# Optimization experiments

Hardware: AMD Instinct MI355X
Metric: run time of the kernel (lower is better)

Reference implementation:

```python
import jax, jax.numpy as jnp
import numpy as np

B, T, C, NH = 8, 512, 512, 8
HD = C // NH

def _layernorm(x, g, b, eps=1e-5):
    mu = jnp.mean(x, axis=-1, keepdims=True)
    var = jnp.var(x, axis=-1, keepdims=True)
    return (x - mu) * jax.lax.rsqrt(var + eps) * g + b

def setup_inputs() -> dict:
    key = jax.random.key(0)
    ks = jax.random.split(key, 5)
    return {
        "x": jax.random.normal(ks[0], (B, T, C), jnp.float32),
        "w_attn": jax.random.normal(ks[1], (3 * C, C), jnp.float32) * (1.0 / np.sqrt(C)),
        "b_attn": jnp.zeros((3 * C,), jnp.float32),
        "w_proj": jax.random.normal(ks[2], (C, C), jnp.float32) * (1.0 / np.sqrt(C)),
        "b_proj": jnp.zeros((C,), jnp.float32),
        "q_gamma": jnp.ones((C,), jnp.float32),
        "q_beta": jnp.zeros((C,), jnp.float32),
        "k_gamma": jnp.ones((C,), jnp.float32),
        "k_beta": jnp.zeros((C,), jnp.float32),
        "rel_emb": jax.random.normal(ks[3], (T, C), jnp.float32) * 0.02,
    }

def reference(x, w_attn, b_attn, w_proj, b_proj, q_gamma, q_beta, k_gamma, k_beta, rel_emb):
    b, t, c = x.shape
    # QKV projection (torch Linear: x @ W.T + b)
    qkv = x @ w_attn.T + b_attn                       # [B,T,3C]
    q, k, v = jnp.split(qkv, 3, axis=-1)
    # per-stream LayerNorm over full embedding dim (q_ln/k_ln = LayerNorm(n_embd))
    q = _layernorm(q, q_gamma, q_beta)
    k = _layernorm(k, k_gamma, k_beta)
    # split heads -> [B,NH,T,HD]
    q = q.reshape(b, t, NH, HD).transpose(0, 2, 1, 3)
    k = k.reshape(b, t, NH, HD).transpose(0, 2, 1, 3)
    v = v.reshape(b, t, NH, HD).transpose(0, 2, 1, 3)
    # relative-position bias: gather rel_emb[|i-j|] -> [T,T,NH,HD]
    idx = jnp.abs(jnp.arange(t)[None, :] - jnp.arange(t)[:, None])  # [T,T] int
    rel = rel_emb[idx].reshape(t, t, NH, HD)
    rel_bias = jnp.einsum("bhqd,qkhd->bhqk", q, rel)  # [B,NH,T,T]
    scale = 1.0 / np.sqrt(HD)
    scores = (jnp.einsum("bhqd,bhkd->bhqk", q, k) + rel_bias) * scale
    causal = jnp.tril(jnp.ones((t, t), bool))
    scores = jnp.where(causal[None, None], scores, jnp.finfo(scores.dtype).min)
    att = jax.nn.softmax(scores, axis=-1)
    y = jnp.einsum("bhqk,bhkd->bhqd", att, v)         # [B,NH,T,HD]
    y = y.transpose(0, 2, 1, 3).reshape(b, t, c)
    return y @ w_proj.T + b_proj
```

## Files before the change

### kernel.cpp

```cpp
#include <hip/hip_runtime.h>
#include <hip/hip_bf16.h>
#include <cstddef>

#define BB 8
#define TT 512
#define CC 512
#define NHH 8
#define HDD 64

typedef __attribute__((ext_vector_type(8))) short short8;
typedef __attribute__((ext_vector_type(4))) float f32x4;

__device__ __forceinline__ unsigned short f2bf(float f) {
    unsigned u = __float_as_uint(f);
    u += 0x7FFFu + ((u >> 16) & 1u);
    return (unsigned short)(u >> 16);
}
__device__ __forceinline__ float bf2f(unsigned short h) {
    return __uint_as_float(((unsigned)h) << 16);
}

__global__ __launch_bounds__(256) void cvt_all_k(
    const float* __restrict__ x, const float* __restrict__ wa,
    const float* __restrict__ wp, const float* __restrict__ rel,
    unsigned short* __restrict__ Xb, unsigned short* __restrict__ Wqb,
    unsigned short* __restrict__ Wpb, unsigned short* __restrict__ Relb)
{
    const int bidx = blockIdx.x;
    const float* in;
    unsigned short* out;
    int base;
    if (bidx < 2048)      { in = x;   out = Xb;   base = bidx; }
    else if (bidx < 2816) { in = wa;  out = Wqb;  base = bidx - 2048; }
    else if (bidx < 3072) { in = wp;  out = Wpb;  base = bidx - 2816; }
    else                  { in = rel; out = Relb; base = bidx - 3072; }
    const int i = base * 1024 + threadIdx.x * 4;
    const float4 v = *(const float4*)(in + i);
    unsigned short tmp[4] = {f2bf(v.x), f2bf(v.y), f2bf(v.z), f2bf(v.w)};
    *(uint2*)(out + i) = *(const uint2*)tmp;
}

__global__ __launch_bounds__(256, 2) void gemm_qkv_mfma(
    const unsigned short* __restrict__ Xb, const unsigned short* __restrict__ Wb,
    const float* __restrict__ bias, unsigned short* __restrict__ qkbuf,
    unsigned short* __restrict__ VT)
{
    __shared__ __align__(16) unsigned short lds[128 * 136];

    const int tid = threadIdx.x;
    const int w = tid >> 6, lane = tid & 63;
    const int c = lane & 15, quad = lane >> 4;
    const int wm = w >> 1, wn = w & 1;
    const int bm = blockIdx.y * 128, bn = blockIdx.x * 128;

    const unsigned short* pp[8];
#pragma unroll
    for (int l = 0; l < 8; ++l) {
        const int ci = w * 8 + l;
        if (ci < 16) {
            const int m16 = ci >> 1, kk = ci & 1;
            pp[l] = Xb + (size_t)(bm + m16 * 16 + c) * 512 + kk * 32 + quad * 8;
        } else {
            const int cb = ci - 16, n16 = cb >> 1, kk = cb & 1;
            pp[l] = Wb + (size_t)(bn + n16 * 16 + c) * 512 + kk * 32 + quad * 8;
        }
    }

    f32x4 acc[4][4];
#pragma unroll
    for (int i = 0; i < 4; ++i)
#pragma unroll
        for (int j = 0; j < 4; ++j) acc[i][j] = (f32x4){0.f, 0.f, 0.f, 0.f};

    short8 pre[8];
#pragma unroll
    for (int l = 0; l < 8; ++l) pre[l] = *(const short8*)pp[l];

    for (int k0 = 0; k0 < 512; k0 += 64) {
        __syncthreads();
#pragma unroll
        for (int l = 0; l < 8; ++l)
            *(short8*)&lds[(w * 8 + l) * 512 + lane * 8] = pre[l];
        __syncthreads();
        if (k0 + 64 < 512) {
#pragma unroll
            for (int l = 0; l < 8; ++l)
                pre[l] = *(const short8*)(pp[l] + k0 + 64);
        }
#pragma unroll
        for (int kk = 0; kk < 2; ++kk) {
            short8 af[4], bfr[4];
#pragma unroll
            for (int i = 0; i < 4; ++i)
                af[i] = *(const short8*)&lds[((wm * 4 + i) * 2 + kk) * 512 + lane * 8];
#pragma unroll
            for (int j = 0; j < 4; ++j)
                bfr[j] = *(const short8*)&lds[(16 + (wn * 4 + j) * 2 + kk) * 512 + lane * 8];
#pragma unroll
            for (int i = 0; i < 4; ++i)
#pragma unroll
                for (int j = 0; j < 4; ++j)
                    acc[i][j] = __builtin_amdgcn_mfma_f32_16x16x32_bf16(
                        af[i], bfr[j], acc[i][j], 0, 0, 0);
        }
    }

    float bj[4];
#pragma unroll
    for (int j = 0; j < 4; ++j) bj[j] = bias[bn + wn * 64 + j * 16 + c];

    if (bn < 1024) {
#pragma unroll
        for (int i = 0; i < 4; ++i)
#pragma unroll
            for (int j = 0; j < 4; ++j) {
                const int n = bn + wn * 64 + j * 16 + c;
#pragma unroll
                for (int r = 0; r < 4; ++r) {
                    const int m = bm + wm * 64 + i * 16 + quad * 4 + r;
                    qkbuf[(size_t)m * 1024 + n] = f2bf(acc[i][j][r] + bj[j]);
                }
            }
    } else {
        __syncthreads();
#pragma unroll
        for (int i = 0; i < 4; ++i)
#pragma unroll
            for (int j = 0; j < 4; ++j) {
                const int col = wn * 64 + j * 16 + c;
                const int row0 = wm * 64 + i * 16 + quad * 4;
                unsigned short t4[4];
#pragma unroll
                for (int r = 0; r < 4; ++r) t4[r] = f2bf(acc[i][j][r] + bj[j]);
                *(uint2*)&lds[col * 136 + row0] = *(const uint2*)t4;
            }
        __syncthreads();
        const int bi = bm >> 9, tb = bm & 511;
        const int hd0 = bn - 1024;
#pragma unroll
        for (int l = 0; l < 8; ++l) {
            const int idx = l * 256 + tid;
            const int col = idx >> 4, grp = idx & 15;
            const short8 v = *(const short8*)&lds[col * 136 + grp * 8];
            const int hd = hd0 + col, h = hd >> 6, d = hd & 63;
            *(short8*)(VT + ((size_t)(bi * NHH + h) * HDD + d) * TT + tb + grp * 8) = v;
        }
    }
}

__global__ __launch_bounds__(256) void ln_k(
    const unsigned short* __restrict__ qkbuf,
    const float* __restrict__ qg, const float* __restrict__ qb,
    const float* __restrict__ kg, const float* __restrict__ kb,
    unsigned short* __restrict__ Qh, unsigned short* __restrict__ Kh)
{
    const int wv = threadIdx.x >> 6, lane = threadIdx.x & 63;
    const int row = blockIdx.x * 4 + wv;
    const int bi = row >> 9, t = row & 511;
    const unsigned short* base = qkbuf + (size_t)row * 1024;

#pragma unroll
    for (int s = 0; s < 2; ++s) {
        const short8 v8 = *(const short8*)(base + s * 512 + lane * 8);
        float vf[8];
#pragma unroll
        for (int i = 0; i < 8; ++i) vf[i] = bf2f(((const unsigned short*)&v8)[i]);
        float sum = 0.f, sq = 0.f;
#pragma unroll
        for (int i = 0; i < 8; ++i) { sum += vf[i]; sq += vf[i] * vf[i]; }
#pragma unroll
        for (int off = 1; off < 64; off <<= 1) {
            sum += __shfl_xor(sum, off);
            sq += __shfl_xor(sq, off);
        }
        const float mu = sum * (1.f / 512.f);
        const float var = sq * (1.f / 512.f) - mu * mu;
        const float rsg = rsqrtf(var + 1e-5f);
        const float* gam = (s ? kg : qg) + lane * 8;
        const float* bet = (s ? kb : qb) + lane * 8;
        const float4 g0 = *(const float4*)gam, g1 = *(const float4*)(gam + 4);
        const float4 b0 = *(const float4*)bet, b1 = *(const float4*)(bet + 4);
        const float gv[8] = {g0.x, g0.y, g0.z, g0.w, g1.x, g1.y, g1.z, g1.w};
        const float bv[8] = {b0.x, b0.y, b0.z, b0.w, b1.x, b1.y, b1.z, b1.w};
        const float osc = s ? 1.0f : 0.125f;
        unsigned short o8[8];
#pragma unroll
        for (int i = 0; i < 8; ++i)
            o8[i] = f2bf(((vf[i] - mu) * rsg * gv[i] + bv[i]) * osc);
        unsigned short* outp = s ? Kh : Qh;
        *(short8*)(outp + ((size_t)(bi * NHH + (lane >> 3)) * TT + t) * HDD
                   + (lane & 7) * 8) = *(const short8*)o8;
    }
}

#define RD_BODY(nr_)                                                            \
    {                                                                           \
        const short8 br0 = *(const short8*)&Rels[((nr_) * 2 + 0) * 512 + lane * 8]; \
        const short8 br1 = *(const short8*)&Rels[((nr_) * 2 + 1) * 512 + lane * 8]; \
        f32x4 a2 = (f32x4){0.f, 0.f, 0.f, 0.f};                                 \
        a2 = __builtin_amdgcn_mfma_f32_16x16x32_bf16(aq0, br0, a2, 0, 0, 0);    \
        a2 = __builtin_amdgcn_mfma_f32_16x16x32_bf16(aq1, br1, a2, 0, 0, 0);    \
        const int colw = (mbase + (nr_) * 16 + c) & 127;                        \
        _Pragma("unroll")                                                       \
        for (int r = 0; r < 4; ++r)                                             \
            RDs[w][(quad * 4 + r) * 132 + colw] = f2bf(a2[r]);                  \
    }

__global__ __launch_bounds__(256, 2) void attn_k(
    const unsigned short* __restrict__ Qh, const unsigned short* __restrict__ Kh,
    const unsigned short* __restrict__ VT, const unsigned short* __restrict__ Relb,
    unsigned short* __restrict__ Yb)
{
    __shared__ __align__(16) unsigned short Ks[8 * 512];
    __shared__ __align__(16) unsigned short Vs[8 * 512];
    __shared__ __align__(16) unsigned short Rels[16 * 512];
    __shared__ __align__(16) unsigned short Ps[4][16 * 72];
    __shared__ __align__(16) unsigned short RDs[4][16 * 132];

    const int tid = threadIdx.x;
    const int w = tid >> 6;
    const int lane = tid & 63;
    const int c = lane & 15;
    const int quad = lane >> 4;

    const int bid = blockIdx.x;
    const int bit0 = bid & 1, bit8 = (bid >> 8) & 1;
    const int s_ = bit0 ^ bit8;
    const int q0 = (bid >> 1) & 7;
    const int qt = s_ ? 7 - q0 : q0;
    const int h = (bid >> 4) & 7;
    const int b = ((bid >> 7) & 1) | (bit8 << 1) | (bit0 << 2);
    const int i0 = qt * 64;

    const unsigned short* Qbase = Qh + (size_t)(b * NHH + h) * TT * HDD;
    const unsigned short* Kbase = Kh + (size_t)(b * NHH + h) * TT * HDD;
    const unsigned short* Vbase = VT + (size_t)(b * NHH + h) * HDD * TT;
    const unsigned short* Rbase = Relb + h * HDD;

    const unsigned short* qp = Qbase + (size_t)(i0 + w * 16 + c) * HDD + quad * 8;
    const short8 aq0 = *(const short8*)qp;
    const short8 aq1 = *(const short8*)(qp + 32);

#pragma unroll
    for (int kk = 0; kk < 2; ++kk) {
        const unsigned short* gp = Kbase + (size_t)(w * 16 + c) * HDD + kk * 32 + quad * 8;
        *(short8*)&Ks[(w * 2 + kk) * 512 + lane * 8] = *(const short8*)gp;
    }
#pragma unroll
    for (int js = 0; js < 2; ++js) {
        const unsigned short* gp = Vbase + (size_t)(w * 16 + c) * TT + js * 32 + quad * 8;
        *(short8*)&Vs[(w * 2 + js) * 512 + lane * 8] = *(const short8*)gp;
    }
    {
        const int mb0 = i0 - 63;
#pragma unroll
        for (int sb = 0; sb < 2; ++sb) {
#pragma unroll
            for (int kk = 0; kk < 2; ++kk) {
                const int n16 = w * 2 + sb;
                int mrow = mb0 + n16 * 16 + c;
                mrow = mrow < 0 ? 0 : (mrow > 511 ? 511 : mrow);
                *(short8*)&Rels[(n16 * 2 + kk) * 512 + lane * 8] =
                    *(const short8*)(Rbase + (size_t)mrow * CC + kk * 32 + quad * 8);
            }
        }
    }

    f32x4 oacc[4];
    float m_i[4], l_i[4];
#pragma unroll
    for (int r = 0; r < 4; ++r) { m_i[r] = -1e30f; l_i[r] = 0.f; }
#pragma unroll
    for (int nd = 0; nd < 4; ++nd) oacc[nd] = (f32x4){0.f, 0.f, 0.f, 0.f};

    __syncthreads();

    for (int jt = 0; jt <= qt; ++jt) {
        const int j0 = jt * 64;

        short8 pK0, pK1, pV0, pV1, pR0, pR1;
        if (jt < qt) {
            const int j1 = j0 + 64;
            const unsigned short* kp = Kbase + (size_t)(j1 + w * 16 + c) * HDD + quad * 8;
            pK0 = *(const short8*)kp;
            pK1 = *(const short8*)(kp + 32);
            const unsigned short* vp = Vbase + (size_t)(w * 16 + c) * TT + j1 + quad * 8;
            pV0 = *(const short8*)vp;
            pV1 = *(const short8*)(vp + 32);
            int mr = i0 - j1 - 63 + w * 16 + c;
            mr = mr < 0 ? 0 : (mr > 511 ? 511 : mr);
            const unsigned short* rp = Rbase + (size_t)mr * CC + quad * 8;
            pR0 = *(const short8*)rp;
            pR1 = *(const short8*)(rp + 32);
        }

        f32x4 sAcc[4];
#pragma unroll
        for (int ns = 0; ns < 4; ++ns) {
            const short8 bk0 = *(const short8*)&Ks[(ns * 2 + 0) * 512 + lane * 8];
            const short8 bk1 = *(const short8*)&Ks[(ns * 2 + 1) * 512 + lane * 8];
            f32x4 a2 = (f32x4){0.f, 0.f, 0.f, 0.f};
            a2 = __builtin_amdgcn_mfma_f32_16x16x32_bf16(aq0, bk0, a2, 0, 0, 0);
            a2 = __builtin_amdgcn_mfma_f32_16x16x32_bf16(aq1, bk1, a2, 0, 0, 0);
            sAcc[ns] = a2;
        }
        const int mbase = i0 - j0 - 63;
        if (jt == 0) {
#pragma unroll
            for (int nr = 0; nr < 8; ++nr) RD_BODY(nr)
        } else {
#pragma unroll
            for (int nr = 0; nr < 4; ++nr) RD_BODY(nr)
        }

        const int dbase = i0 - j0;
        float sc[4][4];
#pragma unroll
        for (int ns = 0; ns < 4; ++ns) {
#pragma unroll
            for (int r = 0; r < 4; ++r) {
                const int r16 = quad * 4 + r;
                const int jc = ns * 16 + c;
                const int dp = (dbase + w * 16 + r16 - jc) & 127;
                const float rdv = bf2f(RDs[w][r16 * 132 + dp]);
                sc[ns][r] = sAcc[ns][r] + rdv;
            }
        }
        if (jt == qt) {
#pragma unroll
            for (int ns = 0; ns < 4; ++ns)
#pragma unroll
                for (int r = 0; r < 4; ++r)
                    if (ns * 16 + c > w * 16 + quad * 4 + r) sc[ns][r] = -1e30f;
        }

        float alpha[4];
#pragma unroll
        for (int r = 0; r < 4; ++r) {
            float m = fmaxf(fmaxf(sc[0][r], sc[1][r]), fmaxf(sc[2][r], sc[3][r]));
#pragma unroll
            for (int off = 1; off < 16; off <<= 1) m = fmaxf(m, __shfl_xor(m, off));
            const float mn = fmaxf(m_i[r], m);
            alpha[r] = __expf(m_i[r] - mn);
            m_i[r] = mn;
        }
        float rs[4] = {0.f, 0.f, 0.f, 0.f};
#pragma unroll
        for (int ns = 0; ns < 4; ++ns) {
#pragma unroll
            for (int r = 0; r < 4; ++r) {
                const float p = __expf(sc[ns][r] - m_i[r]);
                rs[r] += p;
                Ps[w][(quad * 4 + r) * 72 + ns * 16 + c] = f2bf(p);
            }
        }
#pragma unroll
        for (int r = 0; r < 4; ++r) {
#pragma unroll
            for (int off = 1; off < 16; off <<= 1) rs[r] += __shfl_xor(rs[r], off);
            l_i[r] = l_i[r] * alpha[r] + rs[r];
        }
#pragma unroll
        for (int nd = 0; nd < 4; ++nd)
#pragma unroll
            for (int r = 0; r < 4; ++r) oacc[nd][r] *= alpha[r];

        const short8 ap0 = *(const short8*)&Ps[w][c * 72 + 0 * 32 + quad * 8];
        const short8 ap1 = *(const short8*)&Ps[w][c * 72 + 1 * 32 + quad * 8];
#pragma unroll
        for (int nd = 0; nd < 4; ++nd) {
            const short8 bv0 = *(const short8*)&Vs[(nd * 2 + 0) * 512 + lane * 8];
            const short8 bv1 = *(const short8*)&Vs[(nd * 2 + 1) * 512 + lane * 8];
            oacc[nd] = __builtin_amdgcn_mfma_f32_16x16x32_bf16(ap0, bv0, oacc[nd], 0, 0, 0);
            oacc[nd] = __builtin_amdgcn_mfma_f32_16x16x32_bf16(ap1, bv1, oacc[nd], 0, 0, 0);
        }

        if (jt < qt) {
            __syncthreads();
#pragma unroll
            for (int kk = 0; kk < 2; ++kk)
                *(short8*)&Ks[(w * 2 + kk) * 512 + lane * 8] = (kk ? pK1 : pK0);
#pragma unroll
            for (int js = 0; js < 2; ++js)
                *(short8*)&Vs[(w * 2 + js) * 512 + lane * 8] = (js ? pV1 : pV0);
#pragma unroll
            for (int kk = 0; kk < 2; ++kk)
                *(short8*)&Rels[(w * 2 + kk) * 512 + lane * 8] = (kk ? pR1 : pR0);
            __syncthreads();
        }
    }

#pragma unroll
    for (int r = 0; r < 4; ++r) {
        const float inv = 1.f / l_i[r];
        const int trow = i0 + w * 16 + quad * 4 + r;
        unsigned short* yb = Yb + ((size_t)b * TT + trow) * CC + h * HDD;
#pragma unroll
        for (int nd = 0; nd < 4; ++nd)
            yb[nd * 16 + c] = f2bf(oacc[nd][r] * inv);
    }
}

__global__ __launch_bounds__(256, 2) void gemm_proj_mfma(
    const unsigned short* __restrict__ Yb, const unsigned short* __restrict__ Wp,
    const float* __restrict__ bias, float* __restrict__ out)
{
    __shared__ __align__(16) unsigned short lds[24 * 512];

    const int tid = threadIdx.x;
    const int w = tid >> 6, lane = tid & 63;
    const int c = lane & 15, quad = lane >> 4;
    const int wm = w >> 1, wn = w & 1;
    const int bm = blockIdx.y * 64, bn = blockIdx.x * 128;

    const unsigned short* pp[6];
#pragma unroll
    for (int l = 0; l < 6; ++l) {
        const int ci = w * 6 + l;
        if (ci < 8) {
            const int m16 = ci >> 1, kk = ci & 1;
            pp[l] = Yb + (size_t)(bm + m16 * 16 + c) * 512 + kk * 32 + quad * 8;
        } else {
            const int cb = ci - 8, n16 = cb >> 1, kk = cb & 1;
            pp[l] = Wp + (size_t)(bn + n16 * 16 + c) * 512 + kk * 32 + quad * 8;
        }
    }

    f32x4 acc[2][4];
#pragma unroll
    for (int i = 0; i < 2; ++i)
#pragma unroll
        for (int j = 0; j < 4; ++j) acc[i][j] = (f32x4){0.f, 0.f, 0.f, 0.f};

    short8 pre[6];
#pragma unroll
    for (int l = 0; l < 6; ++l) pre[l] = *(const short8*)pp[l];

    for (int k0 = 0; k0 < 512; k0 += 64) {
        __syncthreads();
#pragma unroll
        for (int l = 0; l < 6; ++l)
            *(short8*)&lds[(w * 6 + l) * 512 + lane * 8] = pre[l];
        __syncthreads();
        if (k0 + 64 < 512) {
#pragma unroll
            for (int l = 0; l < 6; ++l)
                pre[l] = *(const short8*)(pp[l] + k0 + 64);
        }
#pragma unroll
        for (int kk = 0; kk < 2; ++kk) {
            short8 af[2], bfr[4];
#pragma unroll
            for (int i = 0; i < 2; ++i)
                af[i] = *(const short8*)&lds[((wm * 2 + i) * 2 + kk) * 512 + lane * 8];
#pragma unroll
            for (int j = 0; j < 4; ++j)
                bfr[j] = *(const short8*)&lds[(8 + (wn * 4 + j) * 2 + kk) * 512 + lane * 8];
#pragma unroll
            for (int i = 0; i < 2; ++i)
#pragma unroll
                for (int j = 0; j < 4; ++j)
                    acc[i][j] = __builtin_amdgcn_mfma_f32_16x16x32_bf16(
                        af[i], bfr[j], acc[i][j], 0, 0, 0);
        }
    }

#pragma unroll
    for (int j = 0; j < 4; ++j) {
        const int n = bn + wn * 64 + j * 16 + c;
        const float bj = bias[n];
#pragma unroll
        for (int i = 0; i < 2; ++i)
#pragma unroll
            for (int r = 0; r < 4; ++r) {
                const int m = bm + wm * 32 + i * 16 + quad * 4 + r;
                out[(size_t)m * 512 + n] = acc[i][j][r] + bj;
            }
    }
}

extern "C" void kernel_launch(void* const* d_in, const int* in_sizes, int n_in,
                              void* d_out, int out_size, void* d_ws, size_t ws_size,
                              hipStream_t stream)
{
    const float* x      = (const float*)d_in[0];
    const float* w_attn = (const float*)d_in[1];
    const float* b_attn = (const float*)d_in[2];
    const float* w_proj = (const float*)d_in[3];
    const float* b_proj = (const float*)d_in[4];
    const float* q_g    = (const float*)d_in[5];
    const float* q_b    = (const float*)d_in[6];
    const float* k_g    = (const float*)d_in[7];
    const float* k_b    = (const float*)d_in[8];
    const float* rel    = (const float*)d_in[9];
    float* out = (float*)d_out;

    unsigned short* qkbuf = (unsigned short*)d_ws;
    unsigned short* Qh   = qkbuf + (size_t)4096 * 1024;
    unsigned short* Kh   = Qh + (size_t)4096 * 512;
    unsigned short* VT   = Kh + (size_t)4096 * 512;
    unsigned short* Relb = VT + (size_t)4096 * 512;
    unsigned short* Xb   = Relb + (size_t)512 * 512;
    unsigned short* Wqb  = Xb + (size_t)4096 * 512;
    unsigned short* Wpb  = Wqb + (size_t)1536 * 512;
    unsigned short* Yb   = qkbuf;

    cvt_all_k<<<3328, 256, 0, stream>>>(x, w_attn, w_proj, rel, Xb, Wqb, Wpb, Relb);
    gemm_qkv_mfma<<<dim3(12, 32), 256, 0, stream>>>(Xb, Wqb, b_attn, qkbuf, VT);
    ln_k<<<1024, 256, 0, stream>>>(qkbuf, q_g, q_b, k_g, k_b, Qh, Kh);
    attn_k<<<512, 256, 0, stream>>>(Qh, Kh, VT, Relb, Yb);
    gemm_proj_mfma<<<dim3(4, 64), 256, 0, stream>>>(Yb, Wpb, b_proj, out);
}
```

Measured before the change: 139.5 us.

## Fuse all stages into one cooperative persistent kernel with grid syncs

Merges the five launches (convert, QKV GEMM, layernorm, attention, projection) into one cooperative kernel of 512 blocks, with grid.sync between stages and a shared LDS buffer reused across stages. The aim is to remove per-launch overhead and the gaps between kernels. It also folds log2(e) into the Q scale so softmax can use exp2f. Risks: grid-wide barriers, idle blocks in stages with fewer tiles, higher register and LDS pressure from one fused kernel, and a fallback path if the cooperative launch fails.

```diff
diff --git a/kernel.cpp b/kernel.cpp
--- a/kernel.cpp
+++ b/kernel.cpp
@@ -1,6 +1,9 @@
 #include <hip/hip_runtime.h>
 #include <hip/hip_bf16.h>
+#include <hip/hip_cooperative_groups.h>
 #include <cstddef>
+
+namespace cg = cooperative_groups;
 
 #define BB 8
 #define TT 512
@@ -20,13 +23,14 @@
     return __uint_as_float(((unsigned)h) << 16);
 }
 
-__global__ __launch_bounds__(256) void cvt_all_k(
+
+__device__ __forceinline__ void cvt_body(
+    int bidx, int tid,
     const float* __restrict__ x, const float* __restrict__ wa,
     const float* __restrict__ wp, const float* __restrict__ rel,
     unsigned short* __restrict__ Xb, unsigned short* __restrict__ Wqb,
     unsigned short* __restrict__ Wpb, unsigned short* __restrict__ Relb)
 {
-    const int bidx = blockIdx.x;
     const float* in;
     unsigned short* out;
     int base;
@@ -34,24 +38,22 @@
     else if (bidx < 2816) { in = wa;  out = Wqb;  base = bidx - 2048; }
     else if (bidx < 3072) { in = wp;  out = Wpb;  base = bidx - 2816; }
     else                  { in = rel; out = Relb; base = bidx - 3072; }
-    const int i = base * 1024 + threadIdx.x * 4;
+    const int i = base * 1024 + tid * 4;
     const float4 v = *(const float4*)(in + i);
     unsigned short tmp[4] = {f2bf(v.x), f2bf(v.y), f2bf(v.z), f2bf(v.w)};
     *(uint2*)(out + i) = *(const uint2*)tmp;
 }
 
-__global__ __launch_bounds__(256, 2) void gemm_qkv_mfma(
+__device__ __forceinline__ void qkv_body(
+    int bx, int by, int tid, unsigned short* __restrict__ lds,
     const unsigned short* __restrict__ Xb, const unsigned short* __restrict__ Wb,
     const float* __restrict__ bias, unsigned short* __restrict__ qkbuf,
     unsigned short* __restrict__ VT)
 {
-    __shared__ __align__(16) unsigned short lds[128 * 136];
-
-    const int tid = threadIdx.x;
     const int w = tid >> 6, lane = tid & 63;
     const int c = lane & 15, quad = lane >> 4;
     const int wm = w >> 1, wn = w & 1;
-    const int bm = blockIdx.y * 128, bn = blockIdx.x * 128;
+    const int bm = by * 128, bn = bx * 128;
 
     const unsigned short* pp[8];
 #pragma unroll
@@ -148,14 +150,15 @@
     }
 }
 
-__global__ __launch_bounds__(256) void ln_k(
+__device__ __forceinline__ void ln_body(
+    int vblk, int tid,
     const unsigned short* __restrict__ qkbuf,
     const float* __restrict__ qg, const float* __restrict__ qb,
     const float* __restrict__ kg, const float* __restrict__ kb,
     unsigned short* __restrict__ Qh, unsigned short* __restrict__ Kh)
 {
-    const int wv = threadIdx.x >> 6, lane = threadIdx.x & 63;
-    const int row = blockIdx.x * 4 + wv;
+    const int wv = tid >> 6, lane = tid & 63;
+    const int row = vblk * 4 + wv;
     const int bi = row >> 9, t = row & 511;
     const unsigned short* base = qkbuf + (size_t)row * 1024;
 
@@ -182,7 +185,7 @@
         const float4 b0 = *(const float4*)bet, b1 = *(const float4*)(bet + 4);
         const float gv[8] = {g0.x, g0.y, g0.z, g0.w, g1.x, g1.y, g1.z, g1.w};
         const float bv[8] = {b0.x, b0.y, b0.z, b0.w, b1.x, b1.y, b1.z, b1.w};
-        const float osc = s ? 1.0f : 0.125f;
+        const float osc = s ? 1.0f : 0.125f * 1.44269504088896f;
         unsigned short o8[8];
 #pragma unroll
         for (int i = 0; i < 8; ++i)
@@ -203,27 +206,26 @@
         const int colw = (mbase + (nr_) * 16 + c) & 127;                        \
         _Pragma("unroll")                                                       \
         for (int r = 0; r < 4; ++r)                                             \
-            RDs[w][(quad * 4 + r) * 132 + colw] = f2bf(a2[r]);                  \
-    }
-
-__global__ __launch_bounds__(256, 2) void attn_k(
+            RDs[w * 2112 + (quad * 4 + r) * 132 + colw] = f2bf(a2[r]);          \
+    }
+
+__device__ __forceinline__ void attn_body(
+    int bid, int tid, unsigned short* __restrict__ sm,
     const unsigned short* __restrict__ Qh, const unsigned short* __restrict__ Kh,
     const unsigned short* __restrict__ VT, const unsigned short* __restrict__ Relb,
     unsigned short* __restrict__ Yb)
 {
-    __shared__ __align__(16) unsigned short Ks[8 * 512];
-    __shared__ __align__(16) unsigned short Vs[8 * 512];
-    __shared__ __align__(16) unsigned short Rels[16 * 512];
-    __shared__ __align__(16) unsigned short Ps[4][16 * 72];
-    __shared__ __align__(16) unsigned short RDs[4][16 * 132];
-
-    const int tid = threadIdx.x;
+    unsigned short* Ks   = sm;
+    unsigned short* Vs   = sm + 4096;
+    unsigned short* Rels = sm + 8192;
+    unsigned short* Ps   = sm + 16384;
+    unsigned short* RDs  = sm + 20992;
+
     const int w = tid >> 6;
     const int lane = tid & 63;
     const int c = lane & 15;
     const int quad = lane >> 4;
 
-    const int bid = blockIdx.x;
     const int bit0 = bid & 1, bit8 = (bid >> 8) & 1;
     const int s_ = bit0 ^ bit8;
     const int q0 = (bid >> 1) & 7;
@@ -322,7 +324,7 @@
                 const int r16 = quad * 4 + r;
                 const int jc = ns * 16 + c;
                 const int dp = (dbase + w * 16 + r16 - jc) & 127;
-                const float rdv = bf2f(RDs[w][r16 * 132 + dp]);
+                const float rdv = bf2f(RDs[w * 2112 + r16 * 132 + dp]);
                 sc[ns][r] = sAcc[ns][r] + rdv;
             }
         }
@@ -341,7 +343,7 @@
 #pragma unroll
             for (int off = 1; off < 16; off <<= 1) m = fmaxf(m, __shfl_xor(m, off));
             const float mn = fmaxf(m_i[r], m);
-            alpha[r] = __expf(m_i[r] - mn);
+            alpha[r] = exp2f(m_i[r] - mn);
             m_i[r] = mn;
         }
         float rs[4] = {0.f, 0.f, 0.f, 0.f};
@@ -349,9 +351,9 @@
         for (int ns = 0; ns < 4; ++ns) {
 #pragma unroll
             for (int r = 0; r < 4; ++r) {
-                const float p = __expf(sc[ns][r] - m_i[r]);
+                const float p = exp2f(sc[ns][r] - m_i[r]);
                 rs[r] += p;
-                Ps[w][(quad * 4 + r) * 72 + ns * 16 + c] = f2bf(p);
+                Ps[w * 1152 + (quad * 4 + r) * 72 + ns * 16 + c] = f2bf(p);
             }
         }
 #pragma unroll
@@ -365,8 +367,8 @@
 #pragma unroll
             for (int r = 0; r < 4; ++r) oacc[nd][r] *= alpha[r];
 
-        const short8 ap0 = *(const short8*)&Ps[w][c * 72 + 0 * 32 + quad * 8];
-        const short8 ap1 = *(const short8*)&Ps[w][c * 72 + 1 * 32 + quad * 8];
+        const short8 ap0 = *(const short8*)&Ps[w * 1152 + c * 72 + 0 * 32 + quad * 8];
+        const short8 ap1 = *(const short8*)&Ps[w * 1152 + c * 72 + 1 * 32 + quad * 8];
 #pragma unroll
         for (int nd = 0; nd < 4; ++nd) {
             const short8 bv0 = *(const short8*)&Vs[(nd * 2 + 0) * 512 + lane * 8];
@@ -401,17 +403,15 @@
     }
 }
 
-__global__ __launch_bounds__(256, 2) void gemm_proj_mfma(
+__device__ __forceinline__ void proj_body(
+    int bx, int by, int tid, unsigned short* __restrict__ lds,
     const unsigned short* __restrict__ Yb, const unsigned short* __restrict__ Wp,
     const float* __restrict__ bias, float* __restrict__ out)
 {
-    __shared__ __align__(16) unsigned short lds[24 * 512];
-
-    const int tid = threadIdx.x;
     const int w = tid >> 6, lane = tid & 63;
     const int c = lane & 15, quad = lane >> 4;
     const int wm = w >> 1, wn = w & 1;
-    const int bm = blockIdx.y * 64, bn = blockIdx.x * 128;
+    const int bm = by * 64, bn = bx * 128;
 
     const unsigned short* pp[6];
 #pragma unroll
@@ -477,6 +477,86 @@
                 out[(size_t)m * 512 + n] = acc[i][j][r] + bj;
             }
     }
+}
+
+__global__ __launch_bounds__(256, 2) void mega_k(
+    const float* __restrict__ x, const float* __restrict__ wa,
+    const float* __restrict__ ba, const float* __restrict__ wp,
+    const float* __restrict__ bp,
+    const float* __restrict__ qg, const float* __restrict__ qb,
+    const float* __restrict__ kg, const float* __restrict__ kb,
+    const float* __restrict__ rel, float* __restrict__ out,
+    unsigned short* __restrict__ qkbuf, unsigned short* __restrict__ Qh,
+    unsigned short* __restrict__ Kh, unsigned short* __restrict__ VT,
+    unsigned short* __restrict__ Relb, unsigned short* __restrict__ Xb,
+    unsigned short* __restrict__ Wqb, unsigned short* __restrict__ Wpb)
+{
+    __shared__ __align__(16) unsigned short SM[29440];
+    cg::grid_group grid = cg::this_grid();
+    const int bid = blockIdx.x;
+    const int tid = threadIdx.x;
+
+    for (int v = bid; v < 3328; v += 512)
+        cvt_body(v, tid, x, wa, wp, rel, Xb, Wqb, Wpb, Relb);
+    grid.sync();
+
+    if (bid < 384)
+        qkv_body(bid % 12, bid / 12, tid, SM, Xb, Wqb, ba, qkbuf, VT);
+    grid.sync();
+
+    for (int v = bid; v < 1024; v += 512)
+        ln_body(v, tid, qkbuf, qg, qb, kg, kb, Qh, Kh);
+    grid.sync();
+
+    attn_body(bid, tid, SM, Qh, Kh, VT, Relb, qkbuf );
+    grid.sync();
+
+    if (bid < 256)
+        proj_body(bid & 3, bid >> 2, tid, SM, qkbuf , Wpb, bp, out);
+}
+
+__global__ __launch_bounds__(256) void cvt_all_k(
+    const float* __restrict__ x, const float* __restrict__ wa,
+    const float* __restrict__ wp, const float* __restrict__ rel,
+    unsigned short* __restrict__ Xb, unsigned short* __restrict__ Wqb,
+    unsigned short* __restrict__ Wpb, unsigned short* __restrict__ Relb)
+{
+    cvt_body(blockIdx.x, threadIdx.x, x, wa, wp, rel, Xb, Wqb, Wpb, Relb);
+}
+
+__global__ __launch_bounds__(256, 2) void gemm_qkv_mfma(
+    const unsigned short* __restrict__ Xb, const unsigned short* __restrict__ Wb,
+    const float* __restrict__ bias, unsigned short* __restrict__ qkbuf,
+    unsigned short* __restrict__ VT)
+{
+    __shared__ __align__(16) unsigned short lds[128 * 136];
+    qkv_body(blockIdx.x, blockIdx.y, threadIdx.x, lds, Xb, Wb, bias, qkbuf, VT);
+}
+
+__global__ __launch_bounds__(256) void ln_k(
+    const unsigned short* __restrict__ qkbuf,
+    const float* __restrict__ qg, const float* __restrict__ qb,
+    const float* __restrict__ kg, const float* __restrict__ kb,
+    unsigned short* __restrict__ Qh, unsigned short* __restrict__ Kh)
+{
+    ln_body(blockIdx.x, threadIdx.x, qkbuf, qg, qb, kg, kb, Qh, Kh);
+}
+
+__global__ __launch_bounds__(256, 2) void attn_k(
+    const unsigned short* __restrict__ Qh, const unsigned short* __restrict__ Kh,
+    const unsigned short* __restrict__ VT, const unsigned short* __restrict__ Relb,
+    unsigned short* __restrict__ Yb)
+{
+    __shared__ __align__(16) unsigned short sm[29440];
+    attn_body(blockIdx.x, threadIdx.x, sm, Qh, Kh, VT, Relb, Yb);
+}
+
+__global__ __launch_bounds__(256, 2) void gemm_proj_mfma(
+    const unsigned short* __restrict__ Yb, const unsigned short* __restrict__ Wp,
+    const float* __restrict__ bias, float* __restrict__ out)
+{
+    __shared__ __align__(16) unsigned short lds[24 * 512];
+    proj_body(blockIdx.x, blockIdx.y, threadIdx.x, lds, Yb, Wp, bias, out);
 }
 
 extern "C" void kernel_launch(void* const* d_in, const int* in_sizes, int n_in,
@@ -505,9 +585,20 @@
     unsigned short* Wpb  = Wqb + (size_t)1536 * 512;
     unsigned short* Yb   = qkbuf;
 
-    cvt_all_k<<<3328, 256, 0, stream>>>(x, w_attn, w_proj, rel, Xb, Wqb, Wpb, Relb);
-    gemm_qkv_mfma<<<dim3(12, 32), 256, 0, stream>>>(Xb, Wqb, b_attn, qkbuf, VT);
-    ln_k<<<1024, 256, 0, stream>>>(qkbuf, q_g, q_b, k_g, k_b, Qh, Kh);
-    attn_k<<<512, 256, 0, stream>>>(Qh, Kh, VT, Relb, Yb);
-    gemm_proj_mfma<<<dim3(4, 64), 256, 0, stream>>>(Yb, Wpb, b_proj, out);
-}
+    void* kargs[] = {
+        (void*)&x, (void*)&w_attn, (void*)&b_attn, (void*)&w_proj,
+        (void*)&b_proj, (void*)&q_g, (void*)&q_b, (void*)&k_g, (void*)&k_b,
+        (void*)&rel, (void*)&out, (void*)&qkbuf, (void*)&Qh, (void*)&Kh,
+        (void*)&VT, (void*)&Relb, (void*)&Xb, (void*)&Wqb, (void*)&Wpb};
+
+    hipError_t err = hipLaunchCooperativeKernel(
+        (const void*)mega_k, dim3(512), dim3(256), kargs, 0, stream);
+
+    if (err != hipSuccess) {
+        cvt_all_k<<<3328, 256, 0, stream>>>(x, w_attn, w_proj, rel, Xb, Wqb, Wpb, Relb);
+        gemm_qkv_mfma<<<dim3(12, 32), 256, 0, stream>>>(Xb, Wqb, b_attn, qkbuf, VT);
+        ln_k<<<1024, 256, 0, stream>>>(qkbuf, q_g, q_b, k_g, k_b, Qh, Kh);
+        attn_k<<<512, 256, 0, stream>>>(Qh, Kh, VT, Relb, Yb);
+        gemm_proj_mfma<<<dim3(4, 64), 256, 0, stream>>>(Yb, Wpb, b_proj, out);
+    }
+}
```

Measured after the change: 390.3 us. +179.7%, slower.

## Fuse fp32-to-bf16 conversion into QKV GEMM and LN kernels, use exp2 softmax

Applied to the files above, without the earlier changes.

Removes the standalone conversion kernel. The QKV GEMM now loads fp32 x and w_attn directly and converts them to bf16 while staging into LDS. The w_proj and rel_emb conversions move into the first blocks of the layernorm kernel. The Q scale is multiplied by log2(e) so the softmax can use exp2f instead of __expf. This saves one launch and a bf16 round trip through memory, at the cost of twice the global load bytes and more registers in the GEMM prefetch.

```diff
diff --git a/kernel.cpp b/kernel.cpp
--- a/kernel.cpp
+++ b/kernel.cpp
@@ -20,28 +20,8 @@
     return __uint_as_float(((unsigned)h) << 16);
 }
 
-__global__ __launch_bounds__(256) void cvt_all_k(
-    const float* __restrict__ x, const float* __restrict__ wa,
-    const float* __restrict__ wp, const float* __restrict__ rel,
-    unsigned short* __restrict__ Xb, unsigned short* __restrict__ Wqb,
-    unsigned short* __restrict__ Wpb, unsigned short* __restrict__ Relb)
-{
-    const int bidx = blockIdx.x;
-    const float* in;
-    unsigned short* out;
-    int base;
-    if (bidx < 2048)      { in = x;   out = Xb;   base = bidx; }
-    else if (bidx < 2816) { in = wa;  out = Wqb;  base = bidx - 2048; }
-    else if (bidx < 3072) { in = wp;  out = Wpb;  base = bidx - 2816; }
-    else                  { in = rel; out = Relb; base = bidx - 3072; }
-    const int i = base * 1024 + threadIdx.x * 4;
-    const float4 v = *(const float4*)(in + i);
-    unsigned short tmp[4] = {f2bf(v.x), f2bf(v.y), f2bf(v.z), f2bf(v.w)};
-    *(uint2*)(out + i) = *(const uint2*)tmp;
-}
-
 __global__ __launch_bounds__(256, 2) void gemm_qkv_mfma(
-    const unsigned short* __restrict__ Xb, const unsigned short* __restrict__ Wb,
+    const float* __restrict__ X, const float* __restrict__ W,
     const float* __restrict__ bias, unsigned short* __restrict__ qkbuf,
     unsigned short* __restrict__ VT)
 {
@@ -53,16 +33,16 @@
     const int wm = w >> 1, wn = w & 1;
     const int bm = blockIdx.y * 128, bn = blockIdx.x * 128;
 
-    const unsigned short* pp[8];
+    const float* pp[8];
 #pragma unroll
     for (int l = 0; l < 8; ++l) {
         const int ci = w * 8 + l;
         if (ci < 16) {
             const int m16 = ci >> 1, kk = ci & 1;
-            pp[l] = Xb + (size_t)(bm + m16 * 16 + c) * 512 + kk * 32 + quad * 8;
+            pp[l] = X + (size_t)(bm + m16 * 16 + c) * 512 + kk * 32 + quad * 8;
         } else {
             const int cb = ci - 16, n16 = cb >> 1, kk = cb & 1;
-            pp[l] = Wb + (size_t)(bn + n16 * 16 + c) * 512 + kk * 32 + quad * 8;
+            pp[l] = W + (size_t)(bn + n16 * 16 + c) * 512 + kk * 32 + quad * 8;
         }
     }
 
@@ -72,20 +52,32 @@
 #pragma unroll
         for (int j = 0; j < 4; ++j) acc[i][j] = (f32x4){0.f, 0.f, 0.f, 0.f};
 
-    short8 pre[8];
-#pragma unroll
-    for (int l = 0; l < 8; ++l) pre[l] = *(const short8*)pp[l];
+    f32x4 pre[8][2];
+#pragma unroll
+    for (int l = 0; l < 8; ++l) {
+        pre[l][0] = *(const f32x4*)pp[l];
+        pre[l][1] = *(const f32x4*)(pp[l] + 4);
+    }
 
     for (int k0 = 0; k0 < 512; k0 += 64) {
         __syncthreads();
 #pragma unroll
-        for (int l = 0; l < 8; ++l)
-            *(short8*)&lds[(w * 8 + l) * 512 + lane * 8] = pre[l];
+        for (int l = 0; l < 8; ++l) {
+            unsigned short t8[8];
+#pragma unroll
+            for (int e = 0; e < 4; ++e) {
+                t8[e] = f2bf(pre[l][0][e]);
+                t8[4 + e] = f2bf(pre[l][1][e]);
+            }
+            *(short8*)&lds[(w * 8 + l) * 512 + lane * 8] = *(const short8*)t8;
+        }
         __syncthreads();
         if (k0 + 64 < 512) {
 #pragma unroll
-            for (int l = 0; l < 8; ++l)
-                pre[l] = *(const short8*)(pp[l] + k0 + 64);
+            for (int l = 0; l < 8; ++l) {
+                pre[l][0] = *(const f32x4*)(pp[l] + k0 + 64);
+                pre[l][1] = *(const f32x4*)(pp[l] + k0 + 68);
+            }
         }
 #pragma unroll
         for (int kk = 0; kk < 2; ++kk) {
@@ -152,8 +144,20 @@
     const unsigned short* __restrict__ qkbuf,
     const float* __restrict__ qg, const float* __restrict__ qb,
     const float* __restrict__ kg, const float* __restrict__ kb,
-    unsigned short* __restrict__ Qh, unsigned short* __restrict__ Kh)
+    unsigned short* __restrict__ Qh, unsigned short* __restrict__ Kh,
+    const float* __restrict__ wp, const float* __restrict__ rel,
+    unsigned short* __restrict__ Wpb, unsigned short* __restrict__ Relb)
 {
+    if (blockIdx.x < 512) {
+        const int seg = blockIdx.x & 255;
+        const float* in = (blockIdx.x < 256) ? wp : rel;
+        unsigned short* outp = (blockIdx.x < 256) ? Wpb : Relb;
+        const int i = seg * 1024 + threadIdx.x * 4;
+        const float4 v = *(const float4*)(in + i);
+        unsigned short tmp[4] = {f2bf(v.x), f2bf(v.y), f2bf(v.z), f2bf(v.w)};
+        *(uint2*)(outp + i) = *(const uint2*)tmp;
+    }
+
     const int wv = threadIdx.x >> 6, lane = threadIdx.x & 63;
     const int row = blockIdx.x * 4 + wv;
     const int bi = row >> 9, t = row & 511;
@@ -182,7 +186,7 @@
         const float4 b0 = *(const float4*)bet, b1 = *(const float4*)(bet + 4);
         const float gv[8] = {g0.x, g0.y, g0.z, g0.w, g1.x, g1.y, g1.z, g1.w};
         const float bv[8] = {b0.x, b0.y, b0.z, b0.w, b1.x, b1.y, b1.z, b1.w};
-        const float osc = s ? 1.0f : 0.125f;
+        const float osc = s ? 1.0f : 0.125f * 1.44269504088896f;
         unsigned short o8[8];
 #pragma unroll
         for (int i = 0; i < 8; ++i)
@@ -341,7 +345,7 @@
 #pragma unroll
             for (int off = 1; off < 16; off <<= 1) m = fmaxf(m, __shfl_xor(m, off));
             const float mn = fmaxf(m_i[r], m);
-            alpha[r] = __expf(m_i[r] - mn);
+            alpha[r] = exp2f(m_i[r] - mn);
             m_i[r] = mn;
         }
         float rs[4] = {0.f, 0.f, 0.f, 0.f};
@@ -349,7 +353,7 @@
         for (int ns = 0; ns < 4; ++ns) {
 #pragma unroll
             for (int r = 0; r < 4; ++r) {
-                const float p = __expf(sc[ns][r] - m_i[r]);
+                const float p = exp2f(sc[ns][r] - m_i[r]);
                 rs[r] += p;
                 Ps[w][(quad * 4 + r) * 72 + ns * 16 + c] = f2bf(p);
             }
@@ -500,14 +504,12 @@
     unsigned short* Kh   = Qh + (size_t)4096 * 512;
     unsigned short* VT   = Kh + (size_t)4096 * 512;
     unsigned short* Relb = VT + (size_t)4096 * 512;
-    unsigned short* Xb   = Relb + (size_t)512 * 512;
-    unsigned short* Wqb  = Xb + (size_t)4096 * 512;
-    unsigned short* Wpb  = Wqb + (size_t)1536 * 512;
+    unsigned short* Wpb  = Relb + (size_t)512 * 512;
     unsigned short* Yb   = qkbuf;
 
-    cvt_all_k<<<3328, 256, 0, stream>>>(x, w_attn, w_proj, rel, Xb, Wqb, Wpb, Relb);
-    gemm_qkv_mfma<<<dim3(12, 32), 256, 0, stream>>>(Xb, Wqb, b_attn, qkbuf, VT);
-    ln_k<<<1024, 256, 0, stream>>>(qkbuf, q_g, q_b, k_g, k_b, Qh, Kh);
+    gemm_qkv_mfma<<<dim3(12, 32), 256, 0, stream>>>(x, w_attn, b_attn, qkbuf, VT);
+    ln_k<<<1024, 256, 0, stream>>>(qkbuf, q_g, q_b, k_g, k_b, Qh, Kh,
+                                   w_proj, rel, Wpb, Relb);
     attn_k<<<512, 256, 0, stream>>>(Qh, Kh, VT, Relb, Yb);
     gemm_proj_mfma<<<dim3(4, 64), 256, 0, stream>>>(Yb, Wpb, b_proj, out);
 }
```

Result: slower. 151.5 us (+8.5%).
